# Optimization experiments

Hardware: AMD Instinct MI355X
Metric: run time of the kernel (lower is better)

The kernel has to match this reference:

```python
import jax, jax.numpy as jnp
import numpy as np

B, S, D, H, HD, L, V, FF = 4, 2048, 768, 12, 64, 6, 32000, 3072
EPS = 1e-5


def setup_inputs() -> dict:
    key = jax.random.key(0)
    ks = jax.random.split(key, 12)
    s = 0.02
    return {
        "input_ids": jax.random.randint(ks[0], (B, S), 0, V),
        "emb": jax.random.normal(ks[1], (V, D), jnp.float32) * s,
        "q_w": jax.random.normal(ks[2], (L, D, D), jnp.float32) * s,
        "q_b": jnp.zeros((L, D), jnp.float32),
        "k_w": jax.random.normal(ks[3], (L, D, D), jnp.float32) * s,
        "k_b": jnp.zeros((L, D), jnp.float32),
        "v_w": jax.random.normal(ks[4], (L, D, D), jnp.float32) * s,
        "v_b": jnp.zeros((L, D), jnp.float32),
        "o_w": jax.random.normal(ks[5], (L, D, D), jnp.float32) * s,
        "o_b": jnp.zeros((L, D), jnp.float32),
        "f1_w": jax.random.normal(ks[6], (L, D, FF), jnp.float32) * s,
        "f1_b": jnp.zeros((L, FF), jnp.float32),
        "f2_w": jax.random.normal(ks[7], (L, FF, D), jnp.float32) * s,
        "f2_b": jnp.zeros((L, D), jnp.float32),
        "n1_w": jnp.ones((L, D), jnp.float32),
        "n1_b": jnp.zeros((L, D), jnp.float32),
        "n2_w": jnp.ones((L, D), jnp.float32),
        "n2_b": jnp.zeros((L, D), jnp.float32),
        "fn_w": jnp.ones((D,), jnp.float32),
        "fn_b": jnp.zeros((D,), jnp.float32),
    }


def _ln(x, w, b):
    m = jnp.mean(x, axis=-1, keepdims=True)
    v = jnp.var(x, axis=-1, keepdims=True)
    return (x - m) * jax.lax.rsqrt(v + EPS) * w + b


def _rope(x):
    # x: [B, S, D]; RoPE applied on full embed dim (as in source)
    inv_freq = 1.0 / (10000.0 ** (jnp.arange(0, D, 2, dtype=jnp.float32) / D))
    ang = jnp.arange(x.shape[1], dtype=jnp.float32)[:, None] * inv_freq[None, :]  # [S, D/2]
    cos, sin = jnp.cos(ang), jnp.sin(ang)
    xe, xo = x[..., ::2], x[..., 1::2]
    re = xe * cos - xo * sin
    ro = xo * cos + xe * sin
    return jnp.stack([re, ro], axis=-1).reshape(x.shape)


def _forward(input_ids, emb, q_w, q_b, k_w, k_b, v_w, v_b, o_w, o_b,
             f1_w, f1_b, f2_w, f2_b, n1_w, n1_b, n2_w, n2_b, fn_w, fn_b):
    h = _rope(emb[input_ids])  # [B, S, D]
    scale = 1.0 / np.sqrt(HD)

    def block(h, p):
        (qw, qb, kw, kb, vw, vb, ow, ob, f1w, f1b, f2w, f2b,
         w1, b1, w2, b2) = p
        xn = _ln(h, w1, b1)
        q = (xn @ qw + qb).reshape(B, S, H, HD)
        k = (xn @ kw + kb).reshape(B, S, H, HD)
        v = (xn @ vw + vb).reshape(B, S, H, HD)
        scores = jnp.einsum('bqhd,bkhd->bhqk', q, k) * scale
        attn = jax.nn.softmax(scores, axis=-1)
        ctx = jnp.einsum('bhqk,bkhd->bqhd', attn, v).reshape(B, S, D)
        h = h + (ctx @ ow + ob)
        xn2 = _ln(h, w2, b2)
        ff = jax.nn.gelu(xn2 @ f1w + f1b, approximate=False) @ f2w + f2b
        return h + ff, None

    params = (q_w, q_b, k_w, k_b, v_w, v_b, o_w, o_b,
              f1_w, f1_b, f2_w, f2_b, n1_w, n1_b, n2_w, n2_b)
    h, _ = jax.lax.scan(block, h, params)
    h = _ln(h, fn_w, fn_b)
    return h @ emb.T  # tied output projection: [B, S, V]


def reference(input_ids, emb, q_w, q_b, k_w, k_b, v_w, v_b, o_w, o_b,
              f1_w, f1_b, f2_w, f2_b, n1_w, n1_b, n2_w, n2_b, fn_w, fn_b):
    return _forward(input_ids, emb, q_w, q_b, k_w, k_b, v_w, v_b, o_w, o_b,
                    f1_w, f1_b, f2_w, f2_b, n1_w, n1_b, n2_w, n2_b, fn_w, fn_b)
```

## Files before the change

kernel.cpp:

```cpp
#include <hip/hip_runtime.h>
#include <hip/hip_bf16.h>
#include <cstdint>
#include <cstddef>

#define TB 4
#define TS 2048
#define TD 768
#define TH 12
#define THD 64
#define TL 6
#define TV 32000
#define TFF 3072
#define TT (TB*TS)
#define TQKV 2304

typedef __bf16 bf16_t;
typedef __attribute__((ext_vector_type(8))) __bf16 bf16x8;
typedef __attribute__((ext_vector_type(4))) __bf16 bf16x4;
typedef __attribute__((ext_vector_type(4))) float f32x4;

__device__ __forceinline__ unsigned short f2bf(float f) {
  union { float f; unsigned u; } x; x.f = f;
  unsigned r = x.u + 0x7fffu + ((x.u >> 16) & 1u);
  return (unsigned short)(r >> 16);
}

__device__ __forceinline__ float fexp2(float x) {
  float r; asm("v_exp_f32 %0, %1" : "=v"(r) : "v"(x)); return r;
}

__device__ __forceinline__ void gld_lds16(const void* g, void* l) {
  unsigned loff = (unsigned)(uintptr_t)l;
  __builtin_amdgcn_global_load_lds(
      (const __attribute__((address_space(1))) unsigned int*)(uintptr_t)g,
      (__attribute__((address_space(3))) unsigned int*)(uintptr_t)loff, 16, 0, 0);
}

#define IRFENCE() asm volatile("" ::: "memory")

__global__ void embed_rope(const int* __restrict__ ids, const float* __restrict__ emb,
                           float* __restrict__ h) {
  int t = blockIdx.x;
  int s = t & (TS - 1);
  int id = ids[t];
  const float* row = emb + (size_t)id * TD;
  float* out = h + (size_t)t * TD;
  for (int p = threadIdx.x; p < TD/2; p += blockDim.x) {
    float xe = row[2*p], xo = row[2*p+1];
    float inv = expf(-(float)(2*p) * (9.210340371976184f / (float)TD));
    float ang = (float)s * inv;
    float c = cosf(ang), sn = sinf(ang);
    out[2*p]   = xe*c - xo*sn;
    out[2*p+1] = xo*c + xe*sn;
  }
}

__global__ __launch_bounds__(256) void ln_fwd(const float* __restrict__ x,
                                              const float* __restrict__ w,
                                              const float* __restrict__ b,
                                              unsigned short* __restrict__ y) {
  int row = blockIdx.x;
  const float* xr = x + (size_t)row * TD;
  int tid = threadIdx.x;
  float4 v = {0.f, 0.f, 0.f, 0.f};
  if (tid < 192) v = *(const float4*)(xr + tid*4);
  float s = (v.x+v.y)+(v.z+v.w);
  float q = (v.x*v.x+v.y*v.y)+(v.z*v.z+v.w*v.w);
  for (int o = 32; o; o >>= 1) { s += __shfl_down(s, o); q += __shfl_down(q, o); }
  __shared__ float ss[4], sq[4];
  int wave = tid >> 6, lane = tid & 63;
  if (lane == 0) { ss[wave] = s; sq[wave] = q; }
  __syncthreads();
  s = ss[0]+ss[1]+ss[2]+ss[3];
  q = sq[0]+sq[1]+sq[2]+sq[3];
  float mean = s * (1.0f/TD);
  float var  = q * (1.0f/TD) - mean*mean;
  float rstd = rsqrtf(var + 1e-5f);
  if (tid < 192) {
    const float4 wv = *(const float4*)(w + tid*4);
    const float4 bv = *(const float4*)(b + tid*4);
    ushort4 o4;
    o4.x = f2bf((v.x-mean)*rstd*wv.x + bv.x);
    o4.y = f2bf((v.y-mean)*rstd*wv.y + bv.y);
    o4.z = f2bf((v.z-mean)*rstd*wv.z + bv.z);
    o4.w = f2bf((v.w-mean)*rstd*wv.w + bv.w);
    *(ushort4*)(y + (size_t)row*TD + tid*4) = o4;
  }
}

__global__ __launch_bounds__(256) void transpose_to_bf16(const float* __restrict__ W,
                                                         unsigned short* __restrict__ Wt,
                                                         int K, int N, int row_off,
                                                         size_t lstride) {
  int ntn = N / 64;
  int tk = (blockIdx.x / ntn) * 64;
  int tn = (blockIdx.x % ntn) * 64;
  const float* Wb = W + (size_t)blockIdx.y * K * N;
  unsigned short* Ob = Wt + (size_t)blockIdx.y * lstride;
  __shared__ float tile[64][65];
  int tid = threadIdx.x;
  int c = tid & 63, w = tid >> 6;
  #pragma unroll
  for (int i = 0; i < 16; ++i) {
    int r = i*4 + w;
    tile[r][c] = Wb[(size_t)(tk + r) * N + tn + c];
  }
  __syncthreads();
  #pragma unroll
  for (int i = 0; i < 16; ++i) {
    int r = i*4 + w;
    Ob[(size_t)(row_off + tn + r) * K + tk + c] = f2bf(tile[c][r]);
  }
}

__global__ void pack_qkv_bias(const float* __restrict__ qb, const float* __restrict__ kb,
                              const float* __restrict__ vb, float* __restrict__ out) {
  int lay = blockIdx.x, i = threadIdx.x;
  out[lay*TQKV + i]        = qb[lay*TD + i];
  out[lay*TQKV + TD + i]   = kb[lay*TD + i];
  out[lay*TQKV + 2*TD + i] = vb[lay*TD + i];
}

__global__ __launch_bounds__(256) void transpose_v(const bf16_t* __restrict__ xqkv,
                                                   bf16_t* __restrict__ vt) {
  const int nst = TS/64;
  int st = blockIdx.x % nst;
  int bh = blockIdx.x / nst;
  int b = bh / TH, h = bh % TH;
  const bf16_t* src = xqkv + (size_t)b*TS*TQKV + 2*TD + h*THD;
  bf16_t* dst = vt + (size_t)bh*THD*TS;
  __shared__ bf16_t tile[64][72];
  int t = threadIdx.x;
  int r = t >> 3, c8 = (t & 7) * 8;
  #pragma unroll
  for (int i = 0; i < 2; ++i) {
    int row = i*32 + r;
    bf16x8 val = *(const bf16x8*)(src + (size_t)(st*64 + row)*TQKV + c8);
    #pragma unroll
    for (int j = 0; j < 8; ++j) tile[row][c8+j] = val[j];
  }
  __syncthreads();
  #pragma unroll
  for (int i = 0; i < 2; ++i) {
    int d = i*32 + r;
    bf16x8 val;
    #pragma unroll
    for (int j = 0; j < 8; ++j) val[j] = tile[c8+j][d];
    *(bf16x8*)(dst + (size_t)d*TS + st*64 + c8) = val;
  }
}

__global__ void convert_bf16_k(const float* __restrict__ in, unsigned short* __restrict__ out) {
  size_t i = ((size_t)blockIdx.x * 256 + threadIdx.x) * 4;
  float4 v = *(const float4*)(in + i);
  ushort4 o;
  o.x = f2bf(v.x); o.y = f2bf(v.y); o.z = f2bf(v.z); o.w = f2bf(v.w);
  *(ushort4*)(out + i) = o;
}

template<int MODE>
__global__ __launch_bounds__(256, 2) void gemm_bt(
    const bf16_t* __restrict__ A, const bf16_t* __restrict__ Bt,
    const float* __restrict__ bias, void* __restrict__ out,
    int N, int K, int ntn) {
  __shared__ __align__(16) bf16_t As[2][128*64];
  __shared__ __align__(16) bf16_t Bs[2][128*64];
  const int tid = threadIdx.x;
  const int lane = tid & 63;
  const int wave = tid >> 6;
  const int wm = wave >> 1, wn = wave & 1;
  const int nwg = gridDim.x;
  const int orig = blockIdx.x;
  const int qd = nwg >> 3, rr = nwg & 7;
  const int xcd = orig & 7, sub = orig >> 3;
  const int wg = (xcd < rr ? xcd*(qd+1) : rr*(qd+1) + (xcd-rr)*qd) + sub;
  const int tm = wg / ntn, tn = wg % ntn;
  const bf16_t* Ab = A + (size_t)tm * 128 * K;
  const bf16_t* Bb = Bt + (size_t)tn * 128 * K;
  const int lr = lane >> 3;
  const int lc = ((lane & 7) ^ lr) * 8;
  const int l15 = lane & 15, l4 = lane >> 4;
  const int flip = (l15 & 7) << 3;
  const int NT = K >> 6;
  f32x4 acc[4][4] = {};

#define STAGE(t, buf) do {                                                   \
    _Pragma("unroll")                                                        \
    for (int it = 0; it < 4; ++it) {                                         \
      const int r0 = it*32 + wave*8;                                         \
      gld_lds16(Ab + (size_t)(r0 + lr)*K + (t)*64 + lc, &As[buf][r0*64 + lr*64]); \
      gld_lds16(Bb + (size_t)(r0 + lr)*K + (t)*64 + lc, &Bs[buf][r0*64 + lr*64]); \
    }                                                                        \
  } while (0)

  STAGE(0, 0);
  for (int t = 0; t < NT; ++t) {
    const int cur = t & 1;
    if (t < NT - 1) {
      STAGE(t+1, cur^1);
      asm volatile("s_waitcnt vmcnt(8)" ::: "memory");
    } else {
      asm volatile("s_waitcnt vmcnt(0)" ::: "memory");
    }
    IRFENCE(); __builtin_amdgcn_s_barrier(); IRFENCE();
    #pragma unroll
    for (int kh = 0; kh < 2; ++kh) {
      bf16x8 af[4], bfr[4];
      #pragma unroll
      for (int i = 0; i < 4; ++i)
        af[i] = *(const bf16x8*)&As[cur][(wm*64 + i*16 + l15)*64 + ((kh*32 + l4*8) ^ flip)];
      #pragma unroll
      for (int i = 0; i < 4; ++i)
        bfr[i] = *(const bf16x8*)&Bs[cur][(wn*64 + i*16 + l15)*64 + ((kh*32 + l4*8) ^ flip)];
      #pragma unroll
      for (int mi = 0; mi < 4; ++mi)
        #pragma unroll
        for (int ni = 0; ni < 4; ++ni)
          acc[mi][ni] = __builtin_amdgcn_mfma_f32_16x16x32_bf16(af[mi], bfr[ni], acc[mi][ni], 0, 0, 0);
    }
    IRFENCE(); __builtin_amdgcn_s_barrier(); IRFENCE();
  }
#undef STAGE
  const int rb = tm*128 + wm*64 + l4*4;
  const int cbase = tn*128 + wn*64 + l15;
  #pragma unroll
  for (int mi = 0; mi < 4; ++mi) {
    #pragma unroll
    for (int ni = 0; ni < 4; ++ni) {
      const int c = cbase + ni*16;
      const float bv = (MODE == 3) ? 0.0f : bias[c];
      #pragma unroll
      for (int r = 0; r < 4; ++r) {
        const size_t idx = (size_t)(rb + mi*16 + r) * N + c;
        float vv = acc[mi][ni][r] + bv;
        if (MODE == 0) {
          ((unsigned short*)out)[idx] = f2bf(vv);
        } else if (MODE == 1) {
          vv = 0.5f * vv * (1.0f + erff(vv * 0.70710678118654752f));
          ((unsigned short*)out)[idx] = f2bf(vv);
        } else if (MODE == 2) {
          ((float*)out)[idx] += vv;
        } else {
          ((float*)out)[idx] = vv;
        }
      }
    }
  }
}

__device__ __forceinline__ int lds_half_off(int R, int C) {
  int lin = ((((R >> 4) << 1) | (C >> 5)) << 10) | ((R & 15) << 6) | ((C & 31) << 1);
  return lin ^ (((R >> 3) & 1) << 5);
}

template<int MODE>
__global__ __launch_bounds__(512, 2) void gemm256(
    const bf16_t* __restrict__ A, const bf16_t* __restrict__ Bt,
    const float* __restrict__ bias, void* __restrict__ out,
    int N, int K, int ntn) {
  __shared__ __align__(16) bf16_t lds[2][2][2][8192];
  const int tid = threadIdx.x;
  const int lane = tid & 63;
  const int wave = tid >> 6;
  const int wm = wave >> 2;
  const int wn = wave & 3;
  const int orig = blockIdx.x;
  const int xcd = orig & 7, sub = orig >> 3;
  const int tm = xcd * 4 + (sub & 3);
  const int tn = sub >> 2;
  const bf16_t* Ab = A  + (size_t)tm * 256 * K;
  const bf16_t* Bb = Bt + (size_t)tn * 256 * K;
  const int l15 = lane & 15, l4 = lane >> 4;
  const int s_row = wave*16 + (lane >> 2);
  const int s_col0 = ((lane & 3) * 8) ^ ((lane >= 32) ? 16 : 0);
  const int NT = K >> 6;

  f32x4 acc[2][4][2][2] = {};
  bf16x8 afr[4][2], bfr0[2][2], bfr1[2][2];

#define STAGEH(mat, half, kt, buf) do {                                          \
    const bf16_t* base_ = (mat) ? Bb : Ab;                                       \
    _Pragma("unroll")                                                            \
    for (int j_ = 0; j_ < 2; ++j_)                                               \
      gld_lds16(base_ + (size_t)((half)*128 + s_row)*K + (kt)*64 + j_*32 + s_col0, \
                &lds[buf][mat][half][(wave*2 + j_) * 512]);                      \
  } while (0)
#define RDA(buf, half) do {                                                      \
    _Pragma("unroll")                                                            \
    for (int m4_ = 0; m4_ < 4; ++m4_)                                            \
      _Pragma("unroll")                                                          \
      for (int kh_ = 0; kh_ < 2; ++kh_)                                          \
        afr[m4_][kh_] = *(const bf16x8*)((const char*)&lds[buf][0][half][0] +    \
            lds_half_off(wm*64 + m4_*16 + l15, kh_*32 + l4*8));                  \
  } while (0)
#define RDB(buf, half, dst) do {                                                 \
    _Pragma("unroll")                                                            \
    for (int n2_ = 0; n2_ < 2; ++n2_)                                            \
      _Pragma("unroll")                                                          \
      for (int kh_ = 0; kh_ < 2; ++kh_)                                          \
        dst[n2_][kh_] = *(const bf16x8*)((const char*)&lds[buf][1][half][0] +    \
            lds_half_off(wn*32 + n2_*16 + l15, kh_*32 + l4*8));                  \
  } while (0)
#define MMA(hA, hB, bsrc) do {                                                   \
    __builtin_amdgcn_s_setprio(1);                                               \
    _Pragma("unroll")                                                            \
    for (int m4_ = 0; m4_ < 4; ++m4_)                                            \
      _Pragma("unroll")                                                          \
      for (int n2_ = 0; n2_ < 2; ++n2_)                                          \
        _Pragma("unroll")                                                        \
        for (int kh_ = 0; kh_ < 2; ++kh_)                                        \
          acc[hA][m4_][hB][n2_] = __builtin_amdgcn_mfma_f32_16x16x32_bf16(       \
              afr[m4_][kh_], bsrc[n2_][kh_], acc[hA][m4_][hB][n2_], 0, 0, 0);    \
    __builtin_amdgcn_s_setprio(0);                                               \
  } while (0)
#define WAITV(n)  asm volatile("s_waitcnt vmcnt(" #n ")" ::: "memory")
#define GATE()    do { asm volatile("s_waitcnt lgkmcnt(0)" ::: "memory");        \
                       __builtin_amdgcn_sched_barrier(0); } while (0)
#define BAR()     do { IRFENCE(); __builtin_amdgcn_s_barrier(); IRFENCE(); } while (0)

  STAGEH(0, 0, 0, 0);
  STAGEH(1, 0, 0, 0);
  STAGEH(1, 1, 0, 0);
  STAGEH(0, 1, 0, 0);
  WAITV(4);
  BAR();

  for (int t = 0; t < NT; ++t) {
    const int c = t & 1;
    const bool last = (t == NT - 1);
    RDA(c, 0);
    RDB(c, 0, bfr0);
    if (!last) STAGEH(0, 0, t+1, c^1);
    if (last) WAITV(2); else WAITV(4);
    BAR(); GATE();
    MMA(0, 0, bfr0);
    RDB(c, 1, bfr1);
    if (!last) STAGEH(1, 0, t+1, c^1);
    if (last) WAITV(0); else WAITV(4);
    BAR(); GATE();
    MMA(0, 1, bfr1);
    RDA(c, 1);
    if (!last) STAGEH(1, 1, t+1, c^1);
    BAR(); GATE();
    MMA(1, 0, bfr0);
    if (!last) STAGEH(0, 1, t+1, c^1);
    WAITV(4);
    BAR(); GATE();
    MMA(1, 1, bfr1);
  }

  #pragma unroll
  for (int hA = 0; hA < 2; ++hA)
    #pragma unroll
    for (int m4 = 0; m4 < 4; ++m4) {
      const int row = tm*256 + hA*128 + wm*64 + m4*16 + l4*4;
      #pragma unroll
      for (int hB = 0; hB < 2; ++hB)
        #pragma unroll
        for (int n2 = 0; n2 < 2; ++n2) {
          const int col = tn*256 + hB*128 + wn*32 + n2*16 + l15;
          const float bv = (MODE == 3) ? 0.0f : bias[col];
          #pragma unroll
          for (int r = 0; r < 4; ++r) {
            const size_t idx = (size_t)(row + r) * N + col;
            float vv = acc[hA][m4][hB][n2][r] + bv;
            if (MODE == 0) {
              ((unsigned short*)out)[idx] = f2bf(vv);
            } else if (MODE == 1) {
              vv = 0.5f * vv * (1.0f + erff(vv * 0.70710678118654752f));
              ((unsigned short*)out)[idx] = f2bf(vv);
            } else if (MODE == 2) {
              ((float*)out)[idx] += vv;
            } else {
              ((float*)out)[idx] = vv;
            }
          }
        }
    }
#undef STAGEH
#undef RDA
#undef RDB
#undef MMA
#undef WAITV
#undef GATE
#undef BAR
}

__global__ __launch_bounds__(256) void attn_fwd(
    const bf16_t* __restrict__ xqkv, const bf16_t* __restrict__ vt,
    unsigned short* __restrict__ ctx) {
  __shared__ __align__(16) bf16_t Ks[2][64*64];
  __shared__ __align__(16) bf16_t Vs[2][64*64];
  __shared__ __align__(16) bf16_t pl[4][32*64];
  const int tid = threadIdx.x, lane = tid & 63, wave = tid >> 6;
  const int orig = blockIdx.x;
  const int wg = (orig & 7) * 96 + (orig >> 3);
  const int qb16 = wg & 15;
  const int bh = wg >> 4;
  const int b = bh / TH, h = bh % TH;
  const bf16_t* qp = xqkv + (size_t)b*TS*TQKV + h*THD;
  const bf16_t* kp = xqkv + (size_t)b*TS*TQKV + TD + h*THD;
  const bf16_t* vp = vt + (size_t)bh*THD*TS;
  const int l15 = lane & 15, l4 = lane >> 4;
  const int qrow0 = qb16*128 + wave*32;
  const float C1 = 0.18033688011112042f;
  bf16x8 qf[2][2];
  #pragma unroll
  for (int mi = 0; mi < 2; ++mi)
    #pragma unroll
    for (int kh = 0; kh < 2; ++kh)
      qf[mi][kh] = *(const bf16x8*)(qp + (size_t)(qrow0 + mi*16 + l15)*TQKV + kh*32 + l4*8);
  const int srow = lane >> 3;
  const int scol = ((lane & 7) ^ srow) * 8;
  f32x4 o[2][4] = {};
  float rm[2] = {-1e30f, -1e30f}, rl[2] = {0.0f, 0.0f};
  const int flipw = (l15 & 7) << 3;

  #define STAGE(t, buf) do {                                                     \
    _Pragma("unroll")                                                            \
    for (int i_ = 0; i_ < 2; ++i_) {                                             \
      const int r_ = i_*32 + wave*8;                                             \
      gld_lds16(kp + (size_t)((t)*64 + r_ + srow)*TQKV + scol, &Ks[buf][r_*64]); \
      gld_lds16(vp + (size_t)(r_ + srow)*TS + (t)*64 + scol,   &Vs[buf][r_*64]); \
    }                                                                            \
  } while (0)

  STAGE(0, 0);
  for (int t = 0; t < TS/64; ++t) {
    const int cur = t & 1;
    if (t < TS/64 - 1) {
      STAGE(t+1, cur^1);
      asm volatile("s_waitcnt vmcnt(4)" ::: "memory");
    } else {
      asm volatile("s_waitcnt vmcnt(0)" ::: "memory");
    }
    IRFENCE(); __builtin_amdgcn_s_barrier(); IRFENCE();
    bf16x8 kf[4][2];
    #pragma unroll
    for (int nj = 0; nj < 4; ++nj) {
      const int row = nj*16 + l15;
      const int flip = (row & 7) << 3;
      #pragma unroll
      for (int kh = 0; kh < 2; ++kh)
        kf[nj][kh] = *(const bf16x8*)&Ks[cur][row*64 + ((kh*32 + l4*8) ^ flip)];
    }
    f32x4 st[2][4] = {};
    #pragma unroll
    for (int mi = 0; mi < 2; ++mi)
      #pragma unroll
      for (int nj = 0; nj < 4; ++nj) {
        st[mi][nj] = __builtin_amdgcn_mfma_f32_16x16x32_bf16(kf[nj][0], qf[mi][0], st[mi][nj], 0, 0, 0);
        st[mi][nj] = __builtin_amdgcn_mfma_f32_16x16x32_bf16(kf[nj][1], qf[mi][1], st[mi][nj], 0, 0, 0);
      }
    float mx[2];
    #pragma unroll
    for (int mi = 0; mi < 2; ++mi) {
      float m0 = fmaxf(fmaxf(st[mi][0][0], st[mi][0][1]), fmaxf(st[mi][0][2], st[mi][0][3]));
      float m1 = fmaxf(fmaxf(st[mi][1][0], st[mi][1][1]), fmaxf(st[mi][1][2], st[mi][1][3]));
      float m2 = fmaxf(fmaxf(st[mi][2][0], st[mi][2][1]), fmaxf(st[mi][2][2], st[mi][2][3]));
      float m3 = fmaxf(fmaxf(st[mi][3][0], st[mi][3][1]), fmaxf(st[mi][3][2], st[mi][3][3]));
      float m = fmaxf(fmaxf(m0, m1), fmaxf(m2, m3)) * C1;
      m = fmaxf(m, __shfl_xor(m, 16));
      m = fmaxf(m, __shfl_xor(m, 32));
      mx[mi] = m;
    }
    float worst = fmaxf(mx[0] - rm[0], mx[1] - rm[1]);
    if (!__all(worst <= 11.54f)) {
      #pragma unroll
      for (int mi = 0; mi < 2; ++mi) {
        float mn = fmaxf(rm[mi], mx[mi]);
        float sc = fexp2(rm[mi] - mn);
        rm[mi] = mn;
        rl[mi] *= sc;
        #pragma unroll
        for (int r = 0; r < 4; ++r) {
          float scr = __shfl(sc, l4*4 + r, 16);
          #pragma unroll
          for (int df = 0; df < 4; ++df) o[mi][df][r] *= scr;
        }
      }
    }
    #pragma unroll
    for (int mi = 0; mi < 2; ++mi) {
      float rs = 0.0f;
      #pragma unroll
      for (int nj = 0; nj < 4; ++nj) {
        float p0 = fexp2(st[mi][nj][0]*C1 - rm[mi]);
        float p1 = fexp2(st[mi][nj][1]*C1 - rm[mi]);
        float p2 = fexp2(st[mi][nj][2]*C1 - rm[mi]);
        float p3 = fexp2(st[mi][nj][3]*C1 - rm[mi]);
        rs += (p0+p1)+(p2+p3);
        bf16x4 pk;
        pk[0] = (bf16_t)p0; pk[1] = (bf16_t)p1; pk[2] = (bf16_t)p2; pk[3] = (bf16_t)p3;
        const int colb = (nj*16 + l4*4) ^ flipw;
        *(bf16x4*)(&pl[wave][(mi*16 + l15)*64 + colb]) = pk;
      }
      rs += __shfl_xor(rs, 16);
      rs += __shfl_xor(rs, 32);
      rl[mi] += rs;
    }
    bf16x8 pa[2][2], vf[4][2];
    #pragma unroll
    for (int mi = 0; mi < 2; ++mi) {
      #pragma unroll
      for (int ks = 0; ks < 2; ++ks)
        pa[mi][ks] = *(const bf16x8*)&pl[wave][(mi*16 + l15)*64 + ((ks*32 + l4*8) ^ flipw)];
    }
    #pragma unroll
    for (int df = 0; df < 4; ++df) {
      const int vrow = df*16 + l15;
      const int flip = (vrow & 7) << 3;
      #pragma unroll
      for (int ks = 0; ks < 2; ++ks)
        vf[df][ks] = *(const bf16x8*)&Vs[cur][vrow*64 + ((ks*32 + l4*8) ^ flip)];
    }
    #pragma unroll
    for (int mi = 0; mi < 2; ++mi)
      #pragma unroll
      for (int df = 0; df < 4; ++df) {
        o[mi][df] = __builtin_amdgcn_mfma_f32_16x16x32_bf16(pa[mi][0], vf[df][0], o[mi][df], 0, 0, 0);
        o[mi][df] = __builtin_amdgcn_mfma_f32_16x16x32_bf16(pa[mi][1], vf[df][1], o[mi][df], 0, 0, 0);
      }
    IRFENCE(); __builtin_amdgcn_s_barrier(); IRFENCE();
  }
  #undef STAGE
  #pragma unroll
  for (int mi = 0; mi < 2; ++mi) {
    const float inv = 1.0f / rl[mi];
    #pragma unroll
    for (int r = 0; r < 4; ++r) {
      const float invr = __shfl(inv, l4*4 + r, 16);
      const size_t rowoff = (size_t)b*TS*TD + (size_t)(qrow0 + mi*16 + l4*4 + r)*TD + h*THD;
      #pragma unroll
      for (int df = 0; df < 4; ++df)
        ctx[rowoff + df*16 + l15] = f2bf(o[mi][df][r] * invr);
    }
  }
}

extern "C" void kernel_launch(void* const* d_in, const int* in_sizes, int n_in,
                              void* d_out, int out_size, void* d_ws, size_t ws_size,
                              hipStream_t stream) {
  (void)in_sizes; (void)n_in; (void)out_size;
  const int*   ids  = (const int*)  d_in[0];
  const float* emb  = (const float*)d_in[1];
  const float* q_w  = (const float*)d_in[2];
  const float* q_b  = (const float*)d_in[3];
  const float* k_w  = (const float*)d_in[4];
  const float* k_b  = (const float*)d_in[5];
  const float* v_w  = (const float*)d_in[6];
  const float* v_b  = (const float*)d_in[7];
  const float* o_w  = (const float*)d_in[8];
  const float* o_b  = (const float*)d_in[9];
  const float* f1_w = (const float*)d_in[10];
  const float* f1_b = (const float*)d_in[11];
  const float* f2_w = (const float*)d_in[12];
  const float* f2_b = (const float*)d_in[13];
  const float* n1_w = (const float*)d_in[14];
  const float* n1_b = (const float*)d_in[15];
  const float* n2_w = (const float*)d_in[16];
  const float* n2_b = (const float*)d_in[17];
  const float* fn_w = (const float*)d_in[18];
  const float* fn_b = (const float*)d_in[19];

  char* ws = (char*)d_ws;
  size_t off = 0;
  auto alloc = [&](size_t bytes) -> void* {
    void* p = ws + off;
    off += (bytes + 255) & ~(size_t)255;
    return p;
  };
  float*          h    = (float*)         alloc((size_t)TT*TD*4);
  unsigned short* xn   = (unsigned short*)alloc((size_t)TT*TD*2);
  unsigned short* xqkv = (unsigned short*)alloc((size_t)TT*TQKV*2);
  unsigned short* cb   = (unsigned short*)alloc((size_t)TT*TD*2);
  unsigned short* ffb  = (unsigned short*)alloc((size_t)TT*TFF*2);
  unsigned short* wqkv = (unsigned short*)alloc((size_t)TL*TQKV*TD*2);
  unsigned short* wot  = (unsigned short*)alloc((size_t)TL*TD*TD*2);
  unsigned short* wf1t = (unsigned short*)alloc((size_t)TL*TD*TFF*2);
  unsigned short* wf2t = (unsigned short*)alloc((size_t)TL*TD*TFF*2);
  unsigned short* embb = (unsigned short*)alloc((size_t)TV*TD*2);
  float*          bqkv = (float*)         alloc((size_t)TL*TQKV*4);
  if (off > ws_size) return;
  bf16_t* vt = (bf16_t*)ffb;

  transpose_to_bf16<<<dim3((TD/64)*(TD/64), TL), 256, 0, stream>>>(q_w, wqkv, TD, TD, 0,    (size_t)TQKV*TD);
  transpose_to_bf16<<<dim3((TD/64)*(TD/64), TL), 256, 0, stream>>>(k_w, wqkv, TD, TD, TD,   (size_t)TQKV*TD);
  transpose_to_bf16<<<dim3((TD/64)*(TD/64), TL), 256, 0, stream>>>(v_w, wqkv, TD, TD, 2*TD, (size_t)TQKV*TD);
  transpose_to_bf16<<<dim3((TD/64)*(TD/64), TL), 256, 0, stream>>>(o_w, wot, TD, TD, 0, (size_t)TD*TD);
  transpose_to_bf16<<<dim3((TD/64)*(TFF/64), TL), 256, 0, stream>>>(f1_w, wf1t, TD, TFF, 0, (size_t)TD*TFF);
  transpose_to_bf16<<<dim3((TFF/64)*(TD/64), TL), 256, 0, stream>>>(f2_w, wf2t, TFF, TD, 0, (size_t)TD*TFF);
  pack_qkv_bias<<<TL, TD, 0, stream>>>(q_b, k_b, v_b, bqkv);
  convert_bf16_k<<<(TV*TD)/1024, 256, 0, stream>>>(emb, embb);
  embed_rope<<<TT, 256, 0, stream>>>(ids, emb, h);

  for (int lay = 0; lay < TL; ++lay) {
    ln_fwd<<<TT, 256, 0, stream>>>(h, n1_w + lay*TD, n1_b + lay*TD, xn);
    gemm_bt<0><<<(TT/128)*(TQKV/128), 256, 0, stream>>>((const bf16_t*)xn,
        (const bf16_t*)(wqkv + (size_t)lay*TQKV*TD), bqkv + lay*TQKV, xqkv, TQKV, TD, TQKV/128);
    transpose_v<<<(TS/64)*(TB*TH), 256, 0, stream>>>((const bf16_t*)xqkv, vt);
    attn_fwd<<<TB*TH*(TS/128), 256, 0, stream>>>((const bf16_t*)xqkv, vt, cb);
    gemm_bt<2><<<(TT/128)*(TD/128), 256, 0, stream>>>((const bf16_t*)cb,
        (const bf16_t*)(wot + (size_t)lay*TD*TD), o_b + lay*TD, h, TD, TD, TD/128);
    ln_fwd<<<TT, 256, 0, stream>>>(h, n2_w + lay*TD, n2_b + lay*TD, xn);
    gemm_bt<1><<<(TT/128)*(TFF/128), 256, 0, stream>>>((const bf16_t*)xn,
        (const bf16_t*)(wf1t + (size_t)lay*TD*TFF), f1_b + lay*TFF, ffb, TFF, TD, TFF/128);
    gemm_bt<2><<<(TT/128)*(TD/128), 256, 0, stream>>>((const bf16_t*)ffb,
        (const bf16_t*)(wf2t + (size_t)lay*TD*TFF), f2_b + lay*TD, h, TD, TFF, TD/128);
  }
  ln_fwd<<<TT, 256, 0, stream>>>(h, fn_w, fn_b, xn);
  gemm256<3><<<32*(TV/256), 512, 0, stream>>>((const bf16_t*)xn,
      (const bf16_t*)embb, nullptr, d_out, TV, TD, TV/256);
}
```

Before: 2.508 ms.

## Fuse V transpose into QKV GEMM epilogue and triple-buffer attention K/V loads

Adds a QKV GEMM epilogue mode that writes the V section directly in head-major transposed layout, so the separate transpose_v kernel and its extra read/write pass are removed. The attention kernel moves from double to triple-buffered K/V staging and issues loads two tiles ahead, which drops one barrier per iteration. In exchange, the transposed V stores are 8-byte strided writes, and the extra buffer raises LDS use, which may limit occupancy.

```diff
diff --git a/kernel.cpp b/kernel.cpp
--- a/kernel.cpp
+++ b/kernel.cpp
@@ -121,35 +121,6 @@
   out[lay*TQKV + 2*TD + i] = vb[lay*TD + i];
 }
 
-__global__ __launch_bounds__(256) void transpose_v(const bf16_t* __restrict__ xqkv,
-                                                   bf16_t* __restrict__ vt) {
-  const int nst = TS/64;
-  int st = blockIdx.x % nst;
-  int bh = blockIdx.x / nst;
-  int b = bh / TH, h = bh % TH;
-  const bf16_t* src = xqkv + (size_t)b*TS*TQKV + 2*TD + h*THD;
-  bf16_t* dst = vt + (size_t)bh*THD*TS;
-  __shared__ bf16_t tile[64][72];
-  int t = threadIdx.x;
-  int r = t >> 3, c8 = (t & 7) * 8;
-  #pragma unroll
-  for (int i = 0; i < 2; ++i) {
-    int row = i*32 + r;
-    bf16x8 val = *(const bf16x8*)(src + (size_t)(st*64 + row)*TQKV + c8);
-    #pragma unroll
-    for (int j = 0; j < 8; ++j) tile[row][c8+j] = val[j];
-  }
-  __syncthreads();
-  #pragma unroll
-  for (int i = 0; i < 2; ++i) {
-    int d = i*32 + r;
-    bf16x8 val;
-    #pragma unroll
-    for (int j = 0; j < 8; ++j) val[j] = tile[c8+j][d];
-    *(bf16x8*)(dst + (size_t)d*TS + st*64 + c8) = val;
-  }
-}
-
 __global__ void convert_bf16_k(const float* __restrict__ in, unsigned short* __restrict__ out) {
   size_t i = ((size_t)blockIdx.x * 256 + threadIdx.x) * 4;
   float4 v = *(const float4*)(in + i);
@@ -162,6 +133,7 @@
 __global__ __launch_bounds__(256, 2) void gemm_bt(
     const bf16_t* __restrict__ A, const bf16_t* __restrict__ Bt,
     const float* __restrict__ bias, void* __restrict__ out,
+    void* __restrict__ out2,
     int N, int K, int ntn) {
   __shared__ __align__(16) bf16_t As[2][128*64];
   __shared__ __align__(16) bf16_t Bs[2][128*64];
@@ -223,17 +195,31 @@
 #undef STAGE
   const int rb = tm*128 + wm*64 + l4*4;
   const int cbase = tn*128 + wn*64 + l15;
+  const bool vsec = (MODE == 4) && (tn >= (2*TD)/128);
   #pragma unroll
   for (int mi = 0; mi < 4; ++mi) {
     #pragma unroll
     for (int ni = 0; ni < 4; ++ni) {
       const int c = cbase + ni*16;
       const float bv = (MODE == 3) ? 0.0f : bias[c];
+      if (MODE == 4 && vsec) {
+        const int cc = c - 2*TD;
+        const int hh = cc >> 6, d = cc & 63;
+        const int row0 = rb + mi*16;
+        const int bidx = row0 >> 11, s = row0 & (TS-1);
+        ushort4 o4;
+        o4.x = f2bf(acc[mi][ni][0] + bv);
+        o4.y = f2bf(acc[mi][ni][1] + bv);
+        o4.z = f2bf(acc[mi][ni][2] + bv);
+        o4.w = f2bf(acc[mi][ni][3] + bv);
+        *(ushort4*)((unsigned short*)out2 + ((size_t)(bidx*TH + hh)*THD + d)*TS + s) = o4;
+        continue;
+      }
       #pragma unroll
       for (int r = 0; r < 4; ++r) {
         const size_t idx = (size_t)(rb + mi*16 + r) * N + c;
         float vv = acc[mi][ni][r] + bv;
-        if (MODE == 0) {
+        if (MODE == 0 || MODE == 4) {
           ((unsigned short*)out)[idx] = f2bf(vv);
         } else if (MODE == 1) {
           vv = 0.5f * vv * (1.0f + erff(vv * 0.70710678118654752f));
@@ -389,8 +375,8 @@
 __global__ __launch_bounds__(256) void attn_fwd(
     const bf16_t* __restrict__ xqkv, const bf16_t* __restrict__ vt,
     unsigned short* __restrict__ ctx) {
-  __shared__ __align__(16) bf16_t Ks[2][64*64];
-  __shared__ __align__(16) bf16_t Vs[2][64*64];
+  __shared__ __align__(16) bf16_t Ks[3][64*64];
+  __shared__ __align__(16) bf16_t Vs[3][64*64];
   __shared__ __align__(16) bf16_t pl[4][32*64];
   const int tid = threadIdx.x, lane = tid & 63, wave = tid >> 6;
   const int orig = blockIdx.x;
@@ -426,15 +412,19 @@
   } while (0)
 
   STAGE(0, 0);
+  STAGE(1, 1);
+  int cur = 0;
   for (int t = 0; t < TS/64; ++t) {
-    const int cur = t & 1;
     if (t < TS/64 - 1) {
-      STAGE(t+1, cur^1);
       asm volatile("s_waitcnt vmcnt(4)" ::: "memory");
     } else {
       asm volatile("s_waitcnt vmcnt(0)" ::: "memory");
     }
     IRFENCE(); __builtin_amdgcn_s_barrier(); IRFENCE();
+    if (t + 2 < TS/64) {
+      const int nb = (cur + 2 >= 3) ? cur - 1 : cur + 2;
+      STAGE(t+2, nb);
+    }
     bf16x8 kf[4][2];
     #pragma unroll
     for (int nj = 0; nj < 4; ++nj) {
@@ -521,7 +511,7 @@
         o[mi][df] = __builtin_amdgcn_mfma_f32_16x16x32_bf16(pa[mi][0], vf[df][0], o[mi][df], 0, 0, 0);
         o[mi][df] = __builtin_amdgcn_mfma_f32_16x16x32_bf16(pa[mi][1], vf[df][1], o[mi][df], 0, 0, 0);
       }
-    IRFENCE(); __builtin_amdgcn_s_barrier(); IRFENCE();
+    cur = (cur + 1 >= 3) ? 0 : cur + 1;
   }
   #undef STAGE
   #pragma unroll
@@ -596,17 +586,16 @@
 
   for (int lay = 0; lay < TL; ++lay) {
     ln_fwd<<<TT, 256, 0, stream>>>(h, n1_w + lay*TD, n1_b + lay*TD, xn);
-    gemm_bt<0><<<(TT/128)*(TQKV/128), 256, 0, stream>>>((const bf16_t*)xn,
-        (const bf16_t*)(wqkv + (size_t)lay*TQKV*TD), bqkv + lay*TQKV, xqkv, TQKV, TD, TQKV/128);
-    transpose_v<<<(TS/64)*(TB*TH), 256, 0, stream>>>((const bf16_t*)xqkv, vt);
+    gemm_bt<4><<<(TT/128)*(TQKV/128), 256, 0, stream>>>((const bf16_t*)xn,
+        (const bf16_t*)(wqkv + (size_t)lay*TQKV*TD), bqkv + lay*TQKV, xqkv, vt, TQKV, TD, TQKV/128);
     attn_fwd<<<TB*TH*(TS/128), 256, 0, stream>>>((const bf16_t*)xqkv, vt, cb);
     gemm_bt<2><<<(TT/128)*(TD/128), 256, 0, stream>>>((const bf16_t*)cb,
-        (const bf16_t*)(wot + (size_t)lay*TD*TD), o_b + lay*TD, h, TD, TD, TD/128);
+        (const bf16_t*)(wot + (size_t)lay*TD*TD), o_b + lay*TD, h, nullptr, TD, TD, TD/128);
     ln_fwd<<<TT, 256, 0, stream>>>(h, n2_w + lay*TD, n2_b + lay*TD, xn);
     gemm_bt<1><<<(TT/128)*(TFF/128), 256, 0, stream>>>((const bf16_t*)xn,
-        (const bf16_t*)(wf1t + (size_t)lay*TD*TFF), f1_b + lay*TFF, ffb, TFF, TD, TFF/128);
+        (const bf16_t*)(wf1t + (size_t)lay*TD*TFF), f1_b + lay*TFF, ffb, nullptr, TFF, TD, TFF/128);
     gemm_bt<2><<<(TT/128)*(TD/128), 256, 0, stream>>>((const bf16_t*)ffb,
-        (const bf16_t*)(wf2t + (size_t)lay*TD*TFF), f2_b + lay*TD, h, TD, TFF, TD/128);
+        (const bf16_t*)(wf2t + (size_t)lay*TD*TFF), f2_b + lay*TD, h, nullptr, TD, TFF, TD/128);
   }
   ln_fwd<<<TT, 256, 0, stream>>>(h, fn_w, fn_b, xn);
   gemm256<3><<<32*(TV/256), 512, 0, stream>>>((const bf16_t*)xn,
```

New measurement: 2.495 ms. About the same (-0.5%).
